# Kernel optimization log

Measured on AMD Instinct MI355X. Metric: run time of the kernel, lower is better.

The kernel has to match this reference:

```python
import jax, jax.numpy as jnp
import numpy as np

COS_EPS = 1e-8  # torch F.cosine_similarity eps


def setup_inputs() -> dict:
    key = jax.random.key(0)
    k1, k2 = jax.random.split(key)
    x = jax.random.normal(k1, (8192, 512), dtype=jnp.float32)
    class_logits = jax.random.normal(k2, (8192, 100), dtype=jnp.float32)
    return {"x": x, "class_logits": class_logits}


def reference(x, class_logits):
    N, D = x.shape
    C = class_logits.shape[1]

    # class_logits.clone().detach()
    logits = jax.lax.stop_gradient(class_logits)
    pred = jax.nn.softmax(logits, axis=1)
    max_logit = pred.max(axis=1)          # [N]
    max_cls = pred.argmax(axis=1)         # [N] int

    # graph(): pairwise cosine similarity = normalize rows + gram matmul
    norms = jnp.linalg.norm(x, axis=1, keepdims=True)
    xn = x / jnp.maximum(norms, COS_EPS)
    mat = xn @ xn.T                       # [N, N]

    x_agg = mat @ x + x                   # [N, D]
    x_new = jax.lax.stop_gradient(x_agg)

    # update_prototype: per-class weighted scatter-add then mean over counts
    weighted = x_new * max_logit[:, None]                     # [N, D]
    sums = jax.ops.segment_sum(weighted, max_cls, num_segments=C)      # [C, D]
    counts = jax.ops.segment_sum(jnp.ones((N,), x.dtype), max_cls, num_segments=C)  # [C]
    prototypes = jnp.where(counts[:, None] > 0,
                           sums / jnp.maximum(counts, 1.0)[:, None],
                           jnp.zeros_like(sums))              # [C, D]

    # inter_class_matrix[i, j] = prototypes[j] - prototypes[i]
    inter_class_matrix = prototypes[None, :, :] - prototypes[:, None, :]  # [C, C, D]
    return prototypes, inter_class_matrix
```

## Files before the change

### kernel.cpp

```cpp
#include <hip/hip_runtime.h>
#include <math.h>

#define N_ROWS 8192
#define D_DIM  512
#define C_CLS  100

typedef unsigned short u16;
typedef unsigned int u32;
typedef __attribute__((ext_vector_type(8))) _Float16 half8;
typedef __attribute__((ext_vector_type(4))) float floatx4;

#define WS_G      0
#define WS_INV    262144
#define WS_WV     270336
#define WS_CLS    278528
#define WS_CNT    286720
#define WS_OFFS   286848
#define WS_ORDER  286976
#define WS_U      295168
#define WS_V      346368
#define WS_ZTH    397568

typedef const __attribute__((address_space(1))) u32* gp32;
typedef __attribute__((address_space(3))) u32* lp32;
__device__ __forceinline__ void cp16(const u16* g, u16* l) {
    __builtin_amdgcn_global_load_lds((gp32)g, (lp32)l, 16, 0, 0);
}

__device__ __forceinline__ u16 f2h(float v) {
    _Float16 h = (_Float16)v;
    return *(u16*)&h;
}

__global__ __launch_bounds__(256) void kA(const float* __restrict__ logits,
        const float* __restrict__ x, float* __restrict__ wv, int* __restrict__ cls,
        float* __restrict__ inv, u16* __restrict__ zth, float* __restrict__ G) {
    __shared__ float xs[32 * 516];
    __shared__ float ns[8][32];
    __shared__ float sv_s[32];
    int bx = blockIdx.x, t = threadIdx.x;
    if (bx < 1024) {
        int lane = t & 63;
        int row0 = (bx << 3) + ((t >> 6) << 1);
        #pragma unroll
        for (int rr = 0; rr < 2; ++rr) {
            int row = row0 + rr;
            const float* lrow = logits + (size_t)row * C_CLS;
            float v1 = lrow[lane];
            bool has2 = (lane + 64) < C_CLS;
            float v2 = has2 ? lrow[lane + 64] : -INFINITY;
            float m; int idx;
            if (v2 > v1) { m = v2; idx = lane + 64; } else { m = v1; idx = lane; }
            #pragma unroll
            for (int off = 32; off >= 1; off >>= 1) {
                float om = __shfl_down(m, off);
                int   oi = __shfl_down(idx, off);
                if (om > m || (om == m && oi < idx)) { m = om; idx = oi; }
            }
            m = __shfl(m, 0);
            idx = __shfl(idx, 0);
            float s = expf(v1 - m) + (has2 ? expf(v2 - m) : 0.0f);
            #pragma unroll
            for (int off = 32; off >= 1; off >>= 1) s += __shfl_down(s, off);
            if (lane == 0) {
                wv[row] = 1.0f / s;
                cls[row] = idx;
            }
        }
        return;
    }
    if (bx >= 1280) {
        int i = ((bx - 1280) * 256 + t) * 32;
        float4 z = make_float4(0.f, 0.f, 0.f, 0.f);
        #pragma unroll
        for (int q = 0; q < 8; ++q) *(float4*)&G[i + q * 4] = z;
        return;
    }
    int r0 = (bx - 1024) << 5;
    const float* src = x + (size_t)r0 * D_DIM;
    #pragma unroll
    for (int i = 0; i < 16; ++i) {
        int e = i * 1024 + t * 4;
        int r = e >> 9, c = e & 511;
        *(float4*)&xs[r * 516 + c] = *(const float4*)&src[e];
    }
    __syncthreads();
    {
        int r = t & 31, seg = t >> 5;
        const float* row = &xs[r * 516 + seg * 64];
        float ss = 0.f;
        #pragma unroll
        for (int jj = 0; jj < 64; ++jj) { float v = row[jj]; ss += v * v; }
        ns[seg][r] = ss;
    }
    __syncthreads();
    if (t < 32) {
        float ss = ns[0][t] + ns[1][t] + ns[2][t] + ns[3][t]
                 + ns[4][t] + ns[5][t] + ns[6][t] + ns[7][t];
        float iv = 1.0f / fmaxf(sqrtf(ss), 1e-8f);
        inv[r0 + t] = iv;
        sv_s[t] = sqrtf(iv);
    }
    __syncthreads();
    int c = t >> 2, rq = (t & 3) * 8;
    float svl[8];
    #pragma unroll
    for (int ii = 0; ii < 8; ++ii) svl[ii] = sv_s[rq + ii];
    #pragma unroll
    for (int ct = 0; ct < 8; ++ct) {
        int d = ct * 64 + c;
        u16 o[8];
        #pragma unroll
        for (int ii = 0; ii < 8; ++ii)
            o[ii] = f2h(xs[(rq + ii) * 516 + d] * svl[ii]);
        uint4 val = make_uint4((u32)o[0] | ((u32)o[1] << 16),
                               (u32)o[2] | ((u32)o[3] << 16),
                               (u32)o[4] | ((u32)o[5] << 16),
                               (u32)o[6] | ((u32)o[7] << 16));
        *(uint4*)&zth[(size_t)d * N_ROWS + r0 + rq] = val;
    }
}

__global__ __launch_bounds__(256) void kB(const int* __restrict__ cls,
        int* __restrict__ cnt, int* __restrict__ offs, int* __restrict__ order) {
    __shared__ int hist[128], scan_s[128], cur[128];
    int t = threadIdx.x;
    if (t < 128) hist[t] = 0;
    __syncthreads();
    for (int m = t; m < N_ROWS; m += 256) atomicAdd(&hist[cls[m]], 1);
    __syncthreads();
    if (t < 128) scan_s[t] = hist[t];
    __syncthreads();
    #pragma unroll
    for (int d = 1; d < 128; d <<= 1) {
        int add = (t < 128 && t >= d) ? scan_s[t - d] : 0;
        __syncthreads();
        if (t < 128) scan_s[t] += add;
        __syncthreads();
    }
    if (t < 128) {
        int off0 = scan_s[t] - hist[t];
        cur[t] = off0;
        offs[t] = off0;
        cnt[t] = hist[t];
    }
    __syncthreads();
    for (int m = t; m < N_ROWS; m += 256) {
        int p = atomicAdd(&cur[cls[m]], 1);
        order[p] = m;
    }
}

__global__ __launch_bounds__(256) void kC(const u16* __restrict__ zth,
        const float* __restrict__ x, const float* __restrict__ inv,
        const float* __restrict__ wv, const int* __restrict__ order,
        const int* __restrict__ offs, const int* __restrict__ cnt,
        float* __restrict__ G, float* __restrict__ u_arr, float* __restrict__ v_arr) {
    __shared__ __attribute__((aligned(16))) union {
        struct { u16 Ah[128 * 32], Bh[128 * 32]; } g;
        struct { float us[4][64], vs[4][64]; } uv;
    } sm;
    int bx = blockIdx.x, t = threadIdx.x;
    if (bx >= 160) {
        int idx = bx - 160;
        int c = idx >> 3, jc = idx & 7;
        int g = t >> 6, lane = t & 63;
        int j = jc * 64 + lane;
        int n = cnt[c], o = offs[c];
        float ua = 0.f, va = 0.f;
        for (int p = g; p < n; p += 4) {
            int m = order[o + p];
            float wm = wv[m];
            float wi = wm * inv[m];
            float xv = x[(size_t)m * D_DIM + j];
            ua += wi * xv; va += wm * xv;
        }
        sm.uv.us[g][lane] = ua; sm.uv.vs[g][lane] = va;
        __syncthreads();
        if (g == 0) {
            u_arr[(size_t)c * D_DIM + j] = sm.uv.us[0][lane] + sm.uv.us[1][lane] + sm.uv.us[2][lane] + sm.uv.us[3][lane];
            v_arr[(size_t)c * D_DIM + j] = sm.uv.vs[0][lane] + sm.uv.vs[1][lane] + sm.uv.vs[2][lane] + sm.uv.vs[3][lane];
        }
        return;
    }
    int tile = bx % 10;
    int p = bx / 10;
    int ti = tile < 4 ? 0 : (tile < 7 ? 1 : (tile < 9 ? 2 : 3));
    int tj = tile - (ti == 0 ? 0 : (ti == 1 ? 3 : (ti == 2 ? 5 : 6)));
    int i0 = ti << 7, j0 = tj << 7;
    bool diag = (ti == tj);
    int kb = p << 9;
    int w = t >> 6, l = t & 63;
    int srow = t >> 2, scol = (t & 3) << 3;
    int lm = l & 15, lg = l >> 4;
    floatx4 acc[4][4];
    #pragma unroll
    for (int mi = 0; mi < 4; ++mi)
        #pragma unroll
        for (int ni = 0; ni < 4; ++ni) acc[mi][ni] = (floatx4){0.f, 0.f, 0.f, 0.f};
    int d0 = srow * 32 + scol;
    int d1 = (64 + srow) * 32 + scol;
    const size_t ga0 = (size_t)(i0 + srow) * N_ROWS + kb + scol;
    const size_t ga1 = (size_t)(i0 + 64 + srow) * N_ROWS + kb + scol;
    const size_t gb0 = (size_t)(j0 + srow) * N_ROWS + kb + scol;
    const size_t gb1 = (size_t)(j0 + 64 + srow) * N_ROWS + kb + scol;
    const u16* Bhs = diag ? sm.g.Ah : sm.g.Bh;
    for (int s = 0; s < 16; ++s) {
        int ks = s << 5;
        cp16(zth + ga0 + ks, sm.g.Ah + d0);
        cp16(zth + ga1 + ks, sm.g.Ah + d1);
        if (!diag) {
            cp16(zth + gb0 + ks, sm.g.Bh + d0);
            cp16(zth + gb1 + ks, sm.g.Bh + d1);
        }
        __syncthreads();
        half8 ah[4], bh[4];
        #pragma unroll
        for (int mi = 0; mi < 4; ++mi) {
            int off = (((w & 1) << 6) + (mi << 4) + lm) * 32 + (lg << 3);
            ah[mi] = *(const half8*)&sm.g.Ah[off];
        }
        #pragma unroll
        for (int ni = 0; ni < 4; ++ni) {
            int off = (((w >> 1) << 6) + (ni << 4) + lm) * 32 + (lg << 3);
            bh[ni] = *(const half8*)&Bhs[off];
        }
        #pragma unroll
        for (int mi = 0; mi < 4; ++mi)
            #pragma unroll
            for (int ni = 0; ni < 4; ++ni)
                acc[mi][ni] = __builtin_amdgcn_mfma_f32_16x16x32_f16(ah[mi], bh[ni], acc[mi][ni], 0, 0, 0);
        __syncthreads();
    }
    #pragma unroll
    for (int mi = 0; mi < 4; ++mi) {
        int row0 = i0 + ((w & 1) << 6) + (mi << 4) + (lg << 2);
        #pragma unroll
        for (int ni = 0; ni < 4; ++ni) {
            int col = j0 + ((w >> 1) << 6) + (ni << 4) + lm;
            #pragma unroll
            for (int r = 0; r < 4; ++r) {
                float val = acc[mi][ni][r];
                atomicAdd(&G[(size_t)(row0 + r) * D_DIM + col], val);
                if (!diag)
                    atomicAdd(&G[(size_t)col * D_DIM + (row0 + r)], val);
            }
        }
    }
}

__global__ __launch_bounds__(256) void kD(const float* __restrict__ u_arr,
        const float* __restrict__ v_arr, const int* __restrict__ cnt,
        const float* __restrict__ G, float* __restrict__ out) {
    __shared__ float us[8][512];
    int g = blockIdx.x >> 4;
    int panel = blockIdx.x & 15;
    int t = threadIdx.x;
    for (int idx = t; idx < 8 * 512; idx += 256) {
        int ci = idx >> 9, k = idx & 511;
        int cc = g * 8 + ci;
        us[ci][k] = (cc < C_CLS) ? u_arr[(size_t)cc * D_DIM + k] : 0.f;
    }
    __syncthreads();
    int ci = t >> 5, cj = t & 31;
    int c = g * 8 + ci;
    int j = panel * 32 + cj;
    float acc = 0.f;
    #pragma unroll 8
    for (int k = 0; k < D_DIM; ++k)
        acc += us[ci][k] * G[(size_t)k * D_DIM + j];
    if (c < C_CLS) {
        int n = cnt[c];
        float s = (n > 0) ? 1.0f / (float)n : 0.0f;
        out[(size_t)c * D_DIM + j] = (v_arr[(size_t)c * D_DIM + j] + acc) * s;
    }
}

__global__ __launch_bounds__(256) void kE(const float* __restrict__ proto,
                                          float* __restrict__ inter) {
    int pair = blockIdx.x * 4 + (threadIdx.x >> 6);
    int i = pair / C_CLS;
    int j = pair - i * C_CLS;
    int d = (threadIdx.x & 63) << 3;
    float4 pj0 = *(const float4*)&proto[j * D_DIM + d];
    float4 pj1 = *(const float4*)&proto[j * D_DIM + d + 4];
    float4 pi0 = *(const float4*)&proto[i * D_DIM + d];
    float4 pi1 = *(const float4*)&proto[i * D_DIM + d + 4];
    float4 r0, r1;
    r0.x = pj0.x - pi0.x; r0.y = pj0.y - pi0.y; r0.z = pj0.z - pi0.z; r0.w = pj0.w - pi0.w;
    r1.x = pj1.x - pi1.x; r1.y = pj1.y - pi1.y; r1.z = pj1.z - pi1.z; r1.w = pj1.w - pi1.w;
    *(float4*)&inter[(size_t)pair * D_DIM + d]     = r0;
    *(float4*)&inter[(size_t)pair * D_DIM + d + 4] = r1;
}

extern "C" void kernel_launch(void* const* d_in, const int* in_sizes, int n_in,
                              void* d_out, int out_size, void* d_ws, size_t ws_size,
                              hipStream_t stream) {
    const float* x      = (const float*)d_in[0];
    const float* logits = (const float*)d_in[1];
    float* out = (float*)d_out;
    float* ws  = (float*)d_ws;
    float* G     = ws + WS_G;
    float* inv   = ws + WS_INV;
    float* wv    = ws + WS_WV;
    int*   cls   = (int*)(ws + WS_CLS);
    int*   cnt   = (int*)(ws + WS_CNT);
    int*   offs  = (int*)(ws + WS_OFFS);
    int*   order = (int*)(ws + WS_ORDER);
    float* u_arr = ws + WS_U;
    float* v_arr = ws + WS_V;
    u16* zth = (u16*)(ws + WS_ZTH);

    kA<<<1312, 256, 0, stream>>>(logits, x, wv, cls, inv, zth, G);
    kB<<<1, 256, 0, stream>>>(cls, cnt, offs, order);
    kC<<<960, 256, 0, stream>>>(zth, x, inv, wv, order, offs, cnt, G, u_arr, v_arr);
    kD<<<208, 256, 0, stream>>>(u_arr, v_arr, cnt, G, out);
    kE<<<C_CLS * C_CLS / 4, 256, 0, stream>>>(out, out + C_CLS * D_DIM);
}
```

Before: 173.1 us.

## Replace atomic Gram accumulation with per-split partial tiles and a reduction kernel

The Gram-matrix kernel used to atomically add each 128x128 tile result into G, plus a mirrored transposed add for off-diagonal tiles. It now writes each tile plainly into a per-split partial buffer (16 splits x 10 upper-triangle tiles). A new kernel sums the 16 partials per element, taking the transpose for lower-triangle entries. The G zeroing blocks in the first kernel are dropped. This removes atomic contention and the transposed scattered writes, at the cost of about 10 MB more workspace traffic and one extra launch.

```diff
diff --git a/kernel.cpp b/kernel.cpp
--- a/kernel.cpp
+++ b/kernel.cpp
@@ -11,15 +11,16 @@
 typedef __attribute__((ext_vector_type(4))) float floatx4;
 
 #define WS_G      0
-#define WS_INV    262144
-#define WS_WV     270336
-#define WS_CLS    278528
-#define WS_CNT    286720
-#define WS_OFFS   286848
-#define WS_ORDER  286976
-#define WS_U      295168
-#define WS_V      346368
-#define WS_ZTH    397568
+#define WS_GP     262144
+#define WS_INV    2883584
+#define WS_WV     2891776
+#define WS_CLS    2899968
+#define WS_CNT    2908160
+#define WS_OFFS   2908288
+#define WS_ORDER  2908416
+#define WS_U      2916608
+#define WS_V      2967808
+#define WS_ZTH    3019008
 
 typedef const __attribute__((address_space(1))) u32* gp32;
 typedef __attribute__((address_space(3))) u32* lp32;
@@ -34,7 +35,7 @@
 
 __global__ __launch_bounds__(256) void kA(const float* __restrict__ logits,
         const float* __restrict__ x, float* __restrict__ wv, int* __restrict__ cls,
-        float* __restrict__ inv, u16* __restrict__ zth, float* __restrict__ G) {
+        float* __restrict__ inv, u16* __restrict__ zth) {
     __shared__ float xs[32 * 516];
     __shared__ float ns[8][32];
     __shared__ float sv_s[32];
@@ -69,13 +70,6 @@
         }
         return;
     }
-    if (bx >= 1280) {
-        int i = ((bx - 1280) * 256 + t) * 32;
-        float4 z = make_float4(0.f, 0.f, 0.f, 0.f);
-        #pragma unroll
-        for (int q = 0; q < 8; ++q) *(float4*)&G[i + q * 4] = z;
-        return;
-    }
     int r0 = (bx - 1024) << 5;
     const float* src = x + (size_t)r0 * D_DIM;
     #pragma unroll
@@ -155,7 +149,7 @@
         const float* __restrict__ x, const float* __restrict__ inv,
         const float* __restrict__ wv, const int* __restrict__ order,
         const int* __restrict__ offs, const int* __restrict__ cnt,
-        float* __restrict__ G, float* __restrict__ u_arr, float* __restrict__ v_arr) {
+        float* __restrict__ Gp, float* __restrict__ u_arr, float* __restrict__ v_arr) {
     __shared__ __attribute__((aligned(16))) union {
         struct { u16 Ah[128 * 32], Bh[128 * 32]; } g;
         struct { float us[4][64], vs[4][64]; } uv;
@@ -232,21 +226,32 @@
                 acc[mi][ni] = __builtin_amdgcn_mfma_f32_16x16x32_f16(ah[mi], bh[ni], acc[mi][ni], 0, 0, 0);
         __syncthreads();
     }
+    float* Gb = Gp + ((size_t)(p * 10 + tile) << 14);
     #pragma unroll
     for (int mi = 0; mi < 4; ++mi) {
-        int row0 = i0 + ((w & 1) << 6) + (mi << 4) + (lg << 2);
+        int row0 = ((w & 1) << 6) + (mi << 4) + (lg << 2);
         #pragma unroll
         for (int ni = 0; ni < 4; ++ni) {
-            int col = j0 + ((w >> 1) << 6) + (ni << 4) + lm;
+            int col = ((w >> 1) << 6) + (ni << 4) + lm;
             #pragma unroll
-            for (int r = 0; r < 4; ++r) {
-                float val = acc[mi][ni][r];
-                atomicAdd(&G[(size_t)(row0 + r) * D_DIM + col], val);
-                if (!diag)
-                    atomicAdd(&G[(size_t)col * D_DIM + (row0 + r)], val);
-            }
-        }
-    }
+            for (int r = 0; r < 4; ++r)
+                Gb[(size_t)(row0 + r) * 128 + col] = acc[mi][ni][r];
+        }
+    }
+}
+
+__global__ __launch_bounds__(256) void kR(const float* __restrict__ Gp,
+                                          float* __restrict__ G) {
+    int i = blockIdx.x * 256 + threadIdx.x;
+    int r = i >> 9, c = i & 511;
+    int tr = r >> 7, tc = c >> 7, rr = r & 127, cc = c & 127;
+    if (tr > tc) { int tmp = tr; tr = tc; tc = tmp; tmp = rr; rr = cc; cc = tmp; }
+    int tid = tr * 4 + tc - ((tr * (tr + 1)) >> 1);
+    const float* src = Gp + ((size_t)tid << 14) + rr * 128 + cc;
+    float s = 0.f;
+    #pragma unroll
+    for (int p = 0; p < 16; ++p) s += src[(size_t)p * 163840];
+    G[i] = s;
 }
 
 __global__ __launch_bounds__(256) void kD(const float* __restrict__ u_arr,
@@ -301,6 +306,7 @@
     float* out = (float*)d_out;
     float* ws  = (float*)d_ws;
     float* G     = ws + WS_G;
+    float* Gp    = ws + WS_GP;
     float* inv   = ws + WS_INV;
     float* wv    = ws + WS_WV;
     int*   cls   = (int*)(ws + WS_CLS);
@@ -311,9 +317,10 @@
     float* v_arr = ws + WS_V;
     u16* zth = (u16*)(ws + WS_ZTH);
 
-    kA<<<1312, 256, 0, stream>>>(logits, x, wv, cls, inv, zth, G);
+    kA<<<1280, 256, 0, stream>>>(logits, x, wv, cls, inv, zth);
     kB<<<1, 256, 0, stream>>>(cls, cnt, offs, order);
-    kC<<<960, 256, 0, stream>>>(zth, x, inv, wv, order, offs, cnt, G, u_arr, v_arr);
+    kC<<<960, 256, 0, stream>>>(zth, x, inv, wv, order, offs, cnt, Gp, u_arr, v_arr);
+    kR<<<1024, 256, 0, stream>>>(Gp, G);
     kD<<<208, 256, 0, stream>>>(u_arr, v_arr, cnt, G, out);
     kE<<<C_CLS * C_CLS / 4, 256, 0, stream>>>(out, out + C_CLS * D_DIM);
 }
```

Result: faster. 169.6 us (-2.0%).
